# Performance work log

Hardware: AMD Instinct MI355X
Metric: run time of the kernel (lower is better)

Reference implementation:

```python
import jax, jax.numpy as jnp
import numpy as np
from jax import lax

BATCH, SEQ, IN_DIM, STATE, OUT_DIM = 8, 4096, 256, 256, 256


def setup_inputs() -> dict:
    key = jax.random.key(0)
    kx, ka, kb, kc = jax.random.split(key, 4)
    x = jax.random.normal(kx, (BATCH, SEQ, IN_DIM), dtype=jnp.float32)
    # A initialized as randn normalized by its largest singular value (spectral norm)
    A_init = jax.random.normal(ka, (STATE, STATE), dtype=jnp.float32)
    s_max = jnp.linalg.svd(A_init, compute_uv=False)[0]
    A = A_init / (s_max + 1e-8)
    B = jax.random.normal(kb, (IN_DIM, STATE), dtype=jnp.float32) / IN_DIM
    C = jax.random.normal(kc, (STATE, OUT_DIM), dtype=jnp.float32) / STATE
    h0 = jnp.zeros((STATE,), dtype=jnp.float32)
    return {"x": x, "A": A, "B": B, "C": C, "h0": h0}


def reference(x, A, B, C, h0):
    # h_{t} = h_{t-1} @ A + x_t @ B ;  y_t = h_t @ C
    bsz = x.shape[0]
    xB = jnp.einsum('bsi,in->sbn', x, B)  # precompute input projections, time-major
    h_init = jnp.broadcast_to(h0, (bsz, h0.shape[0]))

    def step(h, xb_t):
        h = h @ A + xb_t
        return h, h

    _, hs = lax.scan(step, h_init, xB)  # hs: [S, B, N]
    y = jnp.einsum('sbn,no->bso', hs, C)  # [B, S, O]
    return y
```

## Files before the change

### kernel.cpp

```cpp
#include <hip/hip_runtime.h>


#define SEQ    4096
#define NBATCH 8
#define ND     256
#define CHUNK  8
#define NCHUNK 512
#define GSZ    16
#define NGRP   32
#define LOSC   2048.0f
#define LOINV  (1.0f/2048.0f)

typedef _Float16 fp16_t;
typedef __attribute__((ext_vector_type(8))) _Float16 f16x8;
typedef __attribute__((ext_vector_type(4))) _Float16 f16x4;
typedef __attribute__((ext_vector_type(4))) float f32x4;

__global__ __launch_bounds__(64) void prep_frags3(
    const float* __restrict__ A, const float* __restrict__ B,
    const float* __restrict__ C,
    fp16_t* __restrict__ fAh, fp16_t* __restrict__ fAl,
    fp16_t* __restrict__ fBh, fp16_t* __restrict__ fBl,
    fp16_t* __restrict__ fCh, fp16_t* __restrict__ fCl) {
  const int which = blockIdx.x >> 7;
  const int blk   = blockIdx.x & 127;
  const float* M = (which == 0) ? A : (which == 1) ? B : C;
  fp16_t* hi = (which == 0) ? fAh : (which == 1) ? fBh : fCh;
  fp16_t* lo = (which == 0) ? fAl : (which == 1) ? fBl : fCl;
  const int lane = threadIdx.x;
  const int tile = blk >> 3, slice = blk & 7;
  const int n  = tile * 16 + (lane & 15);
  const int k0 = slice * 32 + (lane >> 4) * 8;
  f16x8 vh, vl;
  #pragma unroll
  for (int j = 0; j < 8; ++j) {
    const float v = M[(size_t)(k0 + j) * ND + n];
    const fp16_t h = (fp16_t)v;
    vh[j] = h;
    vl[j] = (fp16_t)((v - (float)h) * LOSC);
  }
  const size_t fo = ((size_t)blk * 64 + lane) * 8;
  *(f16x8*)&hi[fo] = vh;
  *(f16x8*)&lo[fo] = vl;
}

__global__ __launch_bounds__(64) void prep_frags2(
    const float* __restrict__ M0, const float* __restrict__ M1,
    fp16_t* __restrict__ h0p, fp16_t* __restrict__ l0p,
    fp16_t* __restrict__ h1p, fp16_t* __restrict__ l1p) {
  const int which = blockIdx.x >> 7;
  const int blk   = blockIdx.x & 127;
  const float* M = (which == 0) ? M0 : M1;
  fp16_t* hi = (which == 0) ? h0p : h1p;
  fp16_t* lo = (which == 0) ? l0p : l1p;
  const int lane = threadIdx.x;
  const int tile = blk >> 3, slice = blk & 7;
  const int n  = tile * 16 + (lane & 15);
  const int k0 = slice * 32 + (lane >> 4) * 8;
  f16x8 vh, vl;
  #pragma unroll
  for (int j = 0; j < 8; ++j) {
    const float v = M[(size_t)(k0 + j) * ND + n];
    const fp16_t h = (fp16_t)v;
    vh[j] = h;
    vl[j] = (fp16_t)((v - (float)h) * LOSC);
  }
  const size_t fo = ((size_t)blk * 64 + lane) * 8;
  *(f16x8*)&hi[fo] = vh;
  *(f16x8*)&lo[fo] = vl;
}

__global__ __launch_bounds__(1024, 2) void mfma_gemm(const float* __restrict__ X,
                                                     const fp16_t* __restrict__ Mhi,
                                                     const fp16_t* __restrict__ Mlo,
                                                     float* __restrict__ Out,
                                                     int mode) {
  const int m0   = blockIdx.x * 64;
  const int tid  = threadIdx.x;
  const int lane = tid & 63;
  const int w    = tid >> 6;
  const int br   = lane & 15;
  const int akg  = lane >> 4;

  __shared__ fp16_t Xh[32 * 512];
  __shared__ fp16_t Xl[32 * 512];
  char* Xhb = (char*)Xh;
  char* Xlb = (char*)Xl;

  #pragma unroll
  for (int pass = 0; pass < 2; ++pass) {
    const int tau = pass * 1024 + tid;
    const int row = tau >> 5;
    const int sub = tau & 31;
    const int s   = sub >> 2;
    const int ak  = sub & 3;
    const int m = m0 + row;
    const size_t in_row = (mode == 0)
        ? ((size_t)(m & 7) * SEQ + (m >> 3))
        : (size_t)m;
    const float* xp = &X[in_row * ND + s * 32 + ak * 8];
    const float4 x0 = *(const float4*)(xp);
    const float4 x1 = *(const float4*)(xp + 4);
    const float a[8] = {x0.x, x0.y, x0.z, x0.w, x1.x, x1.y, x1.z, x1.w};
    f16x8 vh, vl;
    #pragma unroll
    for (int j = 0; j < 8; ++j) {
      const fp16_t h = (fp16_t)a[j];
      vh[j] = h;
      vl[j] = (fp16_t)((a[j] - (float)h) * LOSC);
    }
    const int off = (((row >> 4) * 8 + s) << 10) +
                    (((ak << 4) | (row & 15)) ^ s) * 16;
    *(f16x8*)(Xhb + off) = vh;
    *(f16x8*)(Xlb + off) = vl;
  }

  f16x8 MH[8], ML[8];
  #pragma unroll
  for (int s = 0; s < 8; ++s) {
    const size_t fo = (((size_t)w * 8 + s) * 64 + lane) * 8;
    MH[s] = *(const f16x8*)&Mhi[fo];
    ML[s] = *(const f16x8*)&Mlo[fo];
  }
  __syncthreads();

  f32x4 accm[4], accl[4];
  #pragma unroll
  for (int mt = 0; mt < 4; ++mt) {
    accm[mt] = (f32x4)0.0f;
    accl[mt] = (f32x4)0.0f;
  }

  const int rdslot = (((akg << 4) | br)) * 16;
  #pragma unroll
  for (int s = 0; s < 8; ++s) {
    const int rdoff = (s ^ ((rdslot >> 4) & 0)) ;
    #pragma unroll
    for (int mt = 0; mt < 4; ++mt) {
      const int byte = ((mt * 8 + s) << 10) + ((((akg << 4) | br) ^ s) << 4);
      const f16x8 bh = *(const f16x8*)(Xhb + byte);
      const f16x8 bl = *(const f16x8*)(Xlb + byte);
      accm[mt] = __builtin_amdgcn_mfma_f32_16x16x32_f16(MH[s], bh, accm[mt], 0, 0, 0);
      accl[mt] = __builtin_amdgcn_mfma_f32_16x16x32_f16(ML[s], bh, accl[mt], 0, 0, 0);
      accl[mt] = __builtin_amdgcn_mfma_f32_16x16x32_f16(MH[s], bl, accl[mt], 0, 0, 0);
    }
    (void)rdoff;
  }

  #pragma unroll
  for (int mt = 0; mt < 4; ++mt) {
    const int m = m0 + mt * 16 + br;
    const size_t out_row = (mode == 1)
        ? ((size_t)(m & 7) * SEQ + (m >> 3))
        : (size_t)m;
    float4 o;
    o.x = accm[mt][0] + accl[mt][0] * LOINV;
    o.y = accm[mt][1] + accl[mt][1] * LOINV;
    o.z = accm[mt][2] + accl[mt][2] * LOINV;
    o.w = accm[mt][3] + accl[mt][3] * LOINV;
    *(float4*)&Out[out_row * ND + w * 16 + akg * 4] = o;
  }
}

__global__ __launch_bounds__(1024, 2) void mfma_rscan(
    const fp16_t* __restrict__ Mh, const fp16_t* __restrict__ Ml,
    const float* __restrict__ Init,
    const float* In,
    float* OutEach,
    float* __restrict__ OutFinal,
    int nupd, int gstride, int nseq, int init_bcast, int entry_mode) {
  const int seq0 = blockIdx.x * 2;
  const int tid  = threadIdx.x;
  const int lane = tid & 63;
  const int w    = tid >> 6;
  const int br   = lane & 15;
  const int akg  = lane >> 4;

  __shared__ fp16_t hH[2][8 * 512];
  __shared__ fp16_t hL[2][8 * 512];

  {
    const int task = tid >> 1;
    const int half = tid & 1;
    const int row  = task & 15;
    const int s    = (task >> 4) & 7;
    const int ak   = task >> 7;
    const int sq = seq0 + (row >> 3);
    const int b  = row & 7;
    const int c0 = s * 32 + ak * 8 + half * 4;
    float4 v = make_float4(0.f, 0.f, 0.f, 0.f);
    if (Init != nullptr && sq < nseq) {
      const size_t off = init_bcast ? (size_t)c0
                                    : ((size_t)sq * NBATCH + b) * ND + c0;
      v = *(const float4*)&Init[off];
      if (entry_mode && OutEach != nullptr)
        *(float4*)&OutEach[((size_t)sq * gstride * NBATCH + b) * ND + c0] = v;
    }
    const float a[4] = {v.x, v.y, v.z, v.w};
    f16x4 vh, vl;
    #pragma unroll
    for (int j = 0; j < 4; ++j) {
      const fp16_t h = (fp16_t)a[j];
      vh[j] = h;
      vl[j] = (fp16_t)((a[j] - (float)h) * LOSC);
    }
    const int off = (s << 10) + ((((ak << 4) | row) ^ s) << 4) + half * 8;
    *(f16x4*)((char*)hH[0] + off) = vh;
    *(f16x4*)((char*)hL[0] + off) = vl;
  }

  f16x8 AH[8], AL[8];
  #pragma unroll
  for (int s = 0; s < 8; ++s) {
    const size_t fo = (((size_t)w * 8 + s) * 64 + lane) * 8;
    AH[s] = *(const f16x8*)&Mh[fo];
    AL[s] = *(const f16x8*)&Ml[fo];
  }
  __syncthreads();

  const int sq   = seq0 + (br >> 3);
  const int b    = br & 7;
  const bool live = (sq < nseq);
  const int sqc  = live ? sq : (nseq - 1);
  const int col0 = w * 16 + akg * 4;

  int rdoff[8];
  #pragma unroll
  for (int s = 0; s < 8; ++s)
    rdoff[s] = (s << 10) + ((((akg << 4) | br) ^ s) << 4);
  const int sw   = col0 >> 5;
  const int akr  = (col0 >> 3) & 3;
  const int wroff = (sw << 10) + ((((akr << 4) | br) ^ sw) << 4) + (col0 & 7) * 2;

  float4 uv = *(const float4*)&In[((size_t)(sqc * gstride) * NBATCH + b) * ND + col0];
  float4 uvn;
  f32x4 res;
  int p = 0;
  for (int j = 0; j < nupd; ++j) {
    if (j + 1 < nupd)
      uvn = *(const float4*)&In[((size_t)(sqc * gstride + j + 1) * NBATCH + b) * ND + col0];
    const char* rH = (const char*)hH[p];
    const char* rL = (const char*)hL[p];
    f32x4 accm, acclA, acclB;
    accm[0] = uv.x; accm[1] = uv.y; accm[2] = uv.z; accm[3] = uv.w;
    acclA = (f32x4)0.0f;
    acclB = (f32x4)0.0f;
    #pragma unroll
    for (int s = 0; s < 8; ++s) {
      const f16x8 bh = *(const f16x8*)(rH + rdoff[s]);
      const f16x8 bl = *(const f16x8*)(rL + rdoff[s]);
      accm  = __builtin_amdgcn_mfma_f32_16x16x32_f16(AH[s], bh, accm,  0, 0, 0);
      acclA = __builtin_amdgcn_mfma_f32_16x16x32_f16(AL[s], bh, acclA, 0, 0, 0);
      acclB = __builtin_amdgcn_mfma_f32_16x16x32_f16(AH[s], bl, acclB, 0, 0, 0);
    }
    #pragma unroll
    for (int r = 0; r < 4; ++r) res[r] = accm[r] + (acclA[r] + acclB[r]) * LOINV;
    {
      f16x4 vh, vl;
      #pragma unroll
      for (int r = 0; r < 4; ++r) {
        const fp16_t hh = (fp16_t)res[r];
        vh[r] = hh;
        vl[r] = (fp16_t)((res[r] - (float)hh) * LOSC);
      }
      *(f16x4*)((char*)hH[p ^ 1] + wroff) = vh;
      *(f16x4*)((char*)hL[p ^ 1] + wroff) = vl;
    }
    if (OutEach != nullptr && live) {
      const size_t pos = entry_mode ? (size_t)(sq * gstride + j + 1)
                                    : (size_t)(sq * gstride + j);
      float4 o;
      o.x = res[0]; o.y = res[1]; o.z = res[2]; o.w = res[3];
      *(float4*)&OutEach[(pos * NBATCH + b) * ND + col0] = o;
    }
    uv = uvn;
    p ^= 1;
    __syncthreads();
  }

  if (OutFinal != nullptr && live) {
    float4 o;
    o.x = res[0]; o.y = res[1]; o.z = res[2]; o.w = res[3];
    *(float4*)&OutFinal[((size_t)sq * NBATCH + b) * ND + col0] = o;
  }
}

__global__ __launch_bounds__(256) void gemm256(const float* __restrict__ X,
                                               const float* __restrict__ Y,
                                               float* __restrict__ Out) {
  const int m0 = blockIdx.x * 4;
  const int n  = threadIdx.x;
  __shared__ float Xs[ND][4];
  #pragma unroll
  for (int r = 0; r < 4; ++r) Xs[n][r] = X[(m0 + r) * ND + n];
  __syncthreads();
  float a0 = 0.f, a1 = 0.f, a2 = 0.f, a3 = 0.f;
  #pragma unroll 8
  for (int k = 0; k < ND; ++k) {
    const float yv = Y[k * ND + n];
    const float4 xv = *(const float4*)&Xs[k][0];
    a0 = fmaf(xv.x, yv, a0);
    a1 = fmaf(xv.y, yv, a1);
    a2 = fmaf(xv.z, yv, a2);
    a3 = fmaf(xv.w, yv, a3);
  }
  Out[(m0 + 0) * ND + n] = a0;
  Out[(m0 + 1) * ND + n] = a1;
  Out[(m0 + 2) * ND + n] = a2;
  Out[(m0 + 3) * ND + n] = a3;
}

extern "C" void kernel_launch(void* const* d_in, const int* in_sizes, int n_in,
                              void* d_out, int out_size, void* d_ws, size_t ws_size,
                              hipStream_t stream) {
  const float* x  = (const float*)d_in[0];
  const float* A  = (const float*)d_in[1];
  const float* Bm = (const float*)d_in[2];
  const float* Cm = (const float*)d_in[3];
  const float* h0 = (const float*)d_in[4];
  float* y = (float*)d_out;

  float* U    = (float*)d_ws;
  float* t0   = U + (size_t)SEQ * NBATCH * ND;
  float* t1   = t0 + ND * ND;
  float* A8   = t1 + ND * ND;
  float* A128 = A8 + ND * ND;
  float* E    = A128 + ND * ND;
  float* Sg   = E + (size_t)NCHUNK * NBATCH * ND;
  float* G    = Sg + (size_t)NGRP * NBATCH * ND;
  float* Hc   = G + (size_t)NGRP * NBATCH * ND;
  fp16_t* fA_hi = (fp16_t*)(Hc + (size_t)NCHUNK * NBATCH * ND);
  fp16_t* fA_lo = fA_hi + ND * ND;
  fp16_t* fB_hi = fA_lo + ND * ND;
  fp16_t* fB_lo = fB_hi + ND * ND;
  fp16_t* fC_hi = fB_lo + ND * ND;
  fp16_t* fC_lo = fC_hi + ND * ND;
  fp16_t* fA8_hi   = (fp16_t*)t0;
  fp16_t* fA8_lo   = fA8_hi + ND * ND;
  fp16_t* fA128_hi = (fp16_t*)t1;
  fp16_t* fA128_lo = fA128_hi + ND * ND;

  prep_frags3<<<384, 64, 0, stream>>>(A, Bm, Cm, fA_hi, fA_lo, fB_hi, fB_lo,
                                      fC_hi, fC_lo);

  gemm256<<<64, 256, 0, stream>>>(A,  A,  t0);
  gemm256<<<64, 256, 0, stream>>>(t0, t0, t1);
  gemm256<<<64, 256, 0, stream>>>(t1, t1, A8);
  gemm256<<<64, 256, 0, stream>>>(A8, A8, t0);
  gemm256<<<64, 256, 0, stream>>>(t0, t0, t1);
  gemm256<<<64, 256, 0, stream>>>(t1, t1, t0);
  gemm256<<<64, 256, 0, stream>>>(t0, t0, A128);

  prep_frags2<<<256, 64, 0, stream>>>(A8, A128, fA8_hi, fA8_lo,
                                      fA128_hi, fA128_lo);

  mfma_gemm<<<512, 1024, 0, stream>>>(x, fB_hi, fB_lo, U, 0);

  mfma_rscan<<<NCHUNK / 2, 1024, 0, stream>>>(fA_hi, fA_lo, nullptr, U,
                                              nullptr, E, CHUNK, CHUNK,
                                              NCHUNK, 0, 0);

  mfma_rscan<<<NGRP / 2, 1024, 0, stream>>>(fA8_hi, fA8_lo, nullptr, E,
                                            nullptr, Sg, GSZ, GSZ, NGRP, 0, 0);

  mfma_rscan<<<1, 1024, 0, stream>>>(fA128_hi, fA128_lo, h0, Sg,
                                     G, nullptr, NGRP - 1, NGRP, 1, 1, 1);

  mfma_rscan<<<NGRP / 2, 1024, 0, stream>>>(fA8_hi, fA8_lo, G, E,
                                            Hc, nullptr, GSZ - 1, GSZ, NGRP,
                                            0, 1);

  mfma_rscan<<<NCHUNK / 2, 1024, 0, stream>>>(fA_hi, fA_lo, Hc, U,
                                              U, nullptr, CHUNK, CHUNK,
                                              NCHUNK, 0, 0);

  mfma_gemm<<<512, 1024, 0, stream>>>(U, fC_hi, fC_lo, y, 1);
}
```

Baseline: 232.9 us.

## Fuse input projection into chunk scan and output projection into down-sweep

Replaces the separate x@B GEMM plus first chunk scan with one scan_up kernel that computes each step's input projection with MFMA and immediately feeds the recurrence. Likewise, scan_down merges the final chunk rescan with the y=h@C projection, so hidden states never round-trip to global memory before the output GEMM. This drops two kernel launches and one full U read and write pass. In exchange each block holds twice as many fragment registers (A and B, or A and C), runs at one block per CU, and keeps the serial dependency on the per-step projection.

```diff
diff --git a/kernel.cpp b/kernel.cpp
--- a/kernel.cpp
+++ b/kernel.cpp
@@ -70,95 +70,298 @@
   *(f16x8*)&lo[fo] = vl;
 }
 
-__global__ __launch_bounds__(1024, 2) void mfma_gemm(const float* __restrict__ X,
-                                                     const fp16_t* __restrict__ Mhi,
-                                                     const fp16_t* __restrict__ Mlo,
-                                                     float* __restrict__ Out,
-                                                     int mode) {
-  const int m0   = blockIdx.x * 64;
+__global__ __launch_bounds__(1024, 1) void scan_up(
+    const fp16_t* __restrict__ fAh, const fp16_t* __restrict__ fAl,
+    const fp16_t* __restrict__ fBh, const fp16_t* __restrict__ fBl,
+    const float* __restrict__ x, float* __restrict__ U, float* __restrict__ E) {
+  const int c2   = blockIdx.x;
   const int tid  = threadIdx.x;
   const int lane = tid & 63;
   const int w    = tid >> 6;
   const int br   = lane & 15;
   const int akg  = lane >> 4;
 
-  __shared__ fp16_t Xh[32 * 512];
-  __shared__ fp16_t Xl[32 * 512];
-  char* Xhb = (char*)Xh;
-  char* Xlb = (char*)Xl;
-
-  #pragma unroll
-  for (int pass = 0; pass < 2; ++pass) {
-    const int tau = pass * 1024 + tid;
-    const int row = tau >> 5;
-    const int sub = tau & 31;
-    const int s   = sub >> 2;
-    const int ak  = sub & 3;
-    const int m = m0 + row;
-    const size_t in_row = (mode == 0)
-        ? ((size_t)(m & 7) * SEQ + (m >> 3))
-        : (size_t)m;
-    const float* xp = &X[in_row * ND + s * 32 + ak * 8];
-    const float4 x0 = *(const float4*)(xp);
-    const float4 x1 = *(const float4*)(xp + 4);
-    const float a[8] = {x0.x, x0.y, x0.z, x0.w, x1.x, x1.y, x1.z, x1.w};
-    f16x8 vh, vl;
-    #pragma unroll
-    for (int j = 0; j < 8; ++j) {
-      const fp16_t h = (fp16_t)a[j];
-      vh[j] = h;
-      vl[j] = (fp16_t)((a[j] - (float)h) * LOSC);
-    }
-    const int off = (((row >> 4) * 8 + s) << 10) +
-                    (((ak << 4) | (row & 15)) ^ s) * 16;
-    *(f16x8*)(Xhb + off) = vh;
-    *(f16x8*)(Xlb + off) = vl;
-  }
-
-  f16x8 MH[8], ML[8];
+  __shared__ fp16_t xH[2][8 * 512], xL[2][8 * 512];
+  __shared__ fp16_t hH[2][8 * 512], hL[2][8 * 512];
+
+  const int srow  = tid >> 6;
+  const int scol  = (tid & 63) * 4;
+  const int ss    = (tid >> 3) & 7;
+  const int sak   = (tid >> 1) & 3;
+  const int shalf = tid & 1;
+  const int soff  = (ss << 10) + ((((sak << 4) | srow) ^ ss) << 4) + shalf * 8;
+  const int sb    = srow & 7;
+  const int sc    = 2 * c2 + (srow >> 3);
+  const float* xsrc = &x[((size_t)sb * SEQ + (size_t)sc * CHUNK) * ND + scol];
+
+  f16x8 AH[8], AL[8], BH[8], BL[8];
   #pragma unroll
   for (int s = 0; s < 8; ++s) {
     const size_t fo = (((size_t)w * 8 + s) * 64 + lane) * 8;
-    MH[s] = *(const f16x8*)&Mhi[fo];
-    ML[s] = *(const f16x8*)&Mlo[fo];
+    AH[s] = *(const f16x8*)&fAh[fo];
+    AL[s] = *(const f16x8*)&fAl[fo];
+    BH[s] = *(const f16x8*)&fBh[fo];
+    BL[s] = *(const f16x8*)&fBl[fo];
+  }
+
+  {
+    const float4 xv = *(const float4*)xsrc;
+    const float a[4] = {xv.x, xv.y, xv.z, xv.w};
+    f16x4 vh, vl;
+    #pragma unroll
+    for (int r = 0; r < 4; ++r) {
+      const fp16_t h = (fp16_t)a[r];
+      vh[r] = h;
+      vl[r] = (fp16_t)((a[r] - (float)h) * LOSC);
+    }
+    *(f16x4*)((char*)xH[0] + soff) = vh;
+    *(f16x4*)((char*)xL[0] + soff) = vl;
   }
   __syncthreads();
 
-  f32x4 accm[4], accl[4];
-  #pragma unroll
-  for (int mt = 0; mt < 4; ++mt) {
-    accm[mt] = (f32x4)0.0f;
-    accl[mt] = (f32x4)0.0f;
-  }
-
-  const int rdslot = (((akg << 4) | br)) * 16;
+  const int sq   = 2 * c2 + (br >> 3);
+  const int b    = br & 7;
+  const int col0 = w * 16 + akg * 4;
+  int rdoff[8];
+  #pragma unroll
+  for (int s = 0; s < 8; ++s)
+    rdoff[s] = (s << 10) + ((((akg << 4) | br) ^ s) << 4);
+  const int sw    = col0 >> 5;
+  const int akr   = (col0 >> 3) & 3;
+  const int wroff = (sw << 10) + ((((akr << 4) | br) ^ sw) << 4) + (col0 & 7) * 2;
+
+  f32x4 res;
+  int q = 0, p = 0;
+  #pragma unroll 1
+  for (int j = 0; j < CHUNK; ++j) {
+    float4 xn;
+    if (j + 1 < CHUNK) xn = *(const float4*)(xsrc + (size_t)(j + 1) * ND);
+    f32x4 accm = (f32x4)0.0f, acclA = (f32x4)0.0f, acclB = (f32x4)0.0f;
+    {
+      const char* rH = (const char*)xH[q];
+      const char* rL = (const char*)xL[q];
+      #pragma unroll
+      for (int s = 0; s < 8; ++s) {
+        const f16x8 bh = *(const f16x8*)(rH + rdoff[s]);
+        const f16x8 bl = *(const f16x8*)(rL + rdoff[s]);
+        accm  = __builtin_amdgcn_mfma_f32_16x16x32_f16(BH[s], bh, accm,  0, 0, 0);
+        acclA = __builtin_amdgcn_mfma_f32_16x16x32_f16(BL[s], bh, acclA, 0, 0, 0);
+        acclB = __builtin_amdgcn_mfma_f32_16x16x32_f16(BH[s], bl, acclB, 0, 0, 0);
+      }
+    }
+    {
+      float4 o;
+      o.x = accm[0] + (acclA[0] + acclB[0]) * LOINV;
+      o.y = accm[1] + (acclA[1] + acclB[1]) * LOINV;
+      o.z = accm[2] + (acclA[2] + acclB[2]) * LOINV;
+      o.w = accm[3] + (acclA[3] + acclB[3]) * LOINV;
+      *(float4*)&U[((size_t)(sq * CHUNK + j) * NBATCH + b) * ND + col0] = o;
+    }
+    if (j > 0) {
+      const char* rH = (const char*)hH[p];
+      const char* rL = (const char*)hL[p];
+      #pragma unroll
+      for (int s = 0; s < 8; ++s) {
+        const f16x8 bh = *(const f16x8*)(rH + rdoff[s]);
+        const f16x8 bl = *(const f16x8*)(rL + rdoff[s]);
+        accm  = __builtin_amdgcn_mfma_f32_16x16x32_f16(AH[s], bh, accm,  0, 0, 0);
+        acclA = __builtin_amdgcn_mfma_f32_16x16x32_f16(AL[s], bh, acclA, 0, 0, 0);
+        acclB = __builtin_amdgcn_mfma_f32_16x16x32_f16(AH[s], bl, acclB, 0, 0, 0);
+      }
+    }
+    #pragma unroll
+    for (int r = 0; r < 4; ++r) res[r] = accm[r] + (acclA[r] + acclB[r]) * LOINV;
+    {
+      f16x4 vh, vl;
+      #pragma unroll
+      for (int r = 0; r < 4; ++r) {
+        const fp16_t hh = (fp16_t)res[r];
+        vh[r] = hh;
+        vl[r] = (fp16_t)((res[r] - (float)hh) * LOSC);
+      }
+      *(f16x4*)((char*)hH[p ^ 1] + wroff) = vh;
+      *(f16x4*)((char*)hL[p ^ 1] + wroff) = vl;
+    }
+    if (j + 1 < CHUNK) {
+      const float a[4] = {xn.x, xn.y, xn.z, xn.w};
+      f16x4 vh, vl;
+      #pragma unroll
+      for (int r = 0; r < 4; ++r) {
+        const fp16_t h = (fp16_t)a[r];
+        vh[r] = h;
+        vl[r] = (fp16_t)((a[r] - (float)h) * LOSC);
+      }
+      *(f16x4*)((char*)xH[q ^ 1] + soff) = vh;
+      *(f16x4*)((char*)xL[q ^ 1] + soff) = vl;
+    }
+    q ^= 1; p ^= 1;
+    __syncthreads();
+  }
+  {
+    float4 o;
+    o.x = res[0]; o.y = res[1]; o.z = res[2]; o.w = res[3];
+    *(float4*)&E[((size_t)sq * NBATCH + b) * ND + col0] = o;
+  }
+}
+
+__global__ __launch_bounds__(1024, 1) void scan_down(
+    const fp16_t* __restrict__ fAh, const fp16_t* __restrict__ fAl,
+    const fp16_t* __restrict__ fCh, const fp16_t* __restrict__ fCl,
+    const float* __restrict__ Hc, const float* __restrict__ U,
+    float* __restrict__ y) {
+  const int c2   = blockIdx.x;
+  const int tid  = threadIdx.x;
+  const int lane = tid & 63;
+  const int w    = tid >> 6;
+  const int br   = lane & 15;
+  const int akg  = lane >> 4;
+
+  __shared__ fp16_t hH[2][8 * 512], hL[2][8 * 512];
+
+  {
+    const int srow  = tid >> 6;
+    const int scol  = (tid & 63) * 4;
+    const int ss    = (tid >> 3) & 7;
+    const int sak   = (tid >> 1) & 3;
+    const int shalf = tid & 1;
+    const int soff  = (ss << 10) + ((((sak << 4) | srow) ^ ss) << 4) + shalf * 8;
+    const int sc = 2 * c2 + (srow >> 3);
+    const int sb = srow & 7;
+    const float4 v = *(const float4*)&Hc[((size_t)sc * NBATCH + sb) * ND + scol];
+    const float a[4] = {v.x, v.y, v.z, v.w};
+    f16x4 vh, vl;
+    #pragma unroll
+    for (int r = 0; r < 4; ++r) {
+      const fp16_t h = (fp16_t)a[r];
+      vh[r] = h;
+      vl[r] = (fp16_t)((a[r] - (float)h) * LOSC);
+    }
+    *(f16x4*)((char*)hH[0] + soff) = vh;
+    *(f16x4*)((char*)hL[0] + soff) = vl;
+  }
+
+  f16x8 AH[8], AL[8], CH[8], CL[8];
   #pragma unroll
   for (int s = 0; s < 8; ++s) {
-    const int rdoff = (s ^ ((rdslot >> 4) & 0)) ;
-    #pragma unroll
-    for (int mt = 0; mt < 4; ++mt) {
-      const int byte = ((mt * 8 + s) << 10) + ((((akg << 4) | br) ^ s) << 4);
-      const f16x8 bh = *(const f16x8*)(Xhb + byte);
-      const f16x8 bl = *(const f16x8*)(Xlb + byte);
-      accm[mt] = __builtin_amdgcn_mfma_f32_16x16x32_f16(MH[s], bh, accm[mt], 0, 0, 0);
-      accl[mt] = __builtin_amdgcn_mfma_f32_16x16x32_f16(ML[s], bh, accl[mt], 0, 0, 0);
-      accl[mt] = __builtin_amdgcn_mfma_f32_16x16x32_f16(MH[s], bl, accl[mt], 0, 0, 0);
-    }
-    (void)rdoff;
-  }
-
-  #pragma unroll
-  for (int mt = 0; mt < 4; ++mt) {
-    const int m = m0 + mt * 16 + br;
-    const size_t out_row = (mode == 1)
-        ? ((size_t)(m & 7) * SEQ + (m >> 3))
-        : (size_t)m;
+    const size_t fo = (((size_t)w * 8 + s) * 64 + lane) * 8;
+    AH[s] = *(const f16x8*)&fAh[fo];
+    AL[s] = *(const f16x8*)&fAl[fo];
+    CH[s] = *(const f16x8*)&fCh[fo];
+    CL[s] = *(const f16x8*)&fCl[fo];
+  }
+  __syncthreads();
+
+  const int sq   = 2 * c2 + (br >> 3);
+  const int b    = br & 7;
+  const int col0 = w * 16 + akg * 4;
+  int rdoff[8];
+  #pragma unroll
+  for (int s = 0; s < 8; ++s)
+    rdoff[s] = (s << 10) + ((((akg << 4) | br) ^ s) << 4);
+  const int sw    = col0 >> 5;
+  const int akr   = (col0 >> 3) & 3;
+  const int wroff = (sw << 10) + ((((akr << 4) | br) ^ sw) << 4) + (col0 & 7) * 2;
+  const size_t t0 = (size_t)sq * CHUNK;
+
+  float4 uv = *(const float4*)&U[(t0 * NBATCH + b) * ND + col0];
+  float4 uvn;
+  f32x4 res;
+  int p = 0;
+
+  {
+    uvn = *(const float4*)&U[((t0 + 1) * NBATCH + b) * ND + col0];
+    f32x4 accm, acclA = (f32x4)0.0f, acclB = (f32x4)0.0f;
+    accm[0] = uv.x; accm[1] = uv.y; accm[2] = uv.z; accm[3] = uv.w;
+    const char* rH = (const char*)hH[0];
+    const char* rL = (const char*)hL[0];
+    #pragma unroll
+    for (int s = 0; s < 8; ++s) {
+      const f16x8 bh = *(const f16x8*)(rH + rdoff[s]);
+      const f16x8 bl = *(const f16x8*)(rL + rdoff[s]);
+      accm  = __builtin_amdgcn_mfma_f32_16x16x32_f16(AH[s], bh, accm,  0, 0, 0);
+      acclA = __builtin_amdgcn_mfma_f32_16x16x32_f16(AL[s], bh, acclA, 0, 0, 0);
+      acclB = __builtin_amdgcn_mfma_f32_16x16x32_f16(AH[s], bl, acclB, 0, 0, 0);
+    }
+    #pragma unroll
+    for (int r = 0; r < 4; ++r) res[r] = accm[r] + (acclA[r] + acclB[r]) * LOINV;
+    f16x4 vh, vl;
+    #pragma unroll
+    for (int r = 0; r < 4; ++r) {
+      const fp16_t hh = (fp16_t)res[r];
+      vh[r] = hh;
+      vl[r] = (fp16_t)((res[r] - (float)hh) * LOSC);
+    }
+    *(f16x4*)((char*)hH[1] + wroff) = vh;
+    *(f16x4*)((char*)hL[1] + wroff) = vl;
+    uv = uvn;
+    p = 1;
+    __syncthreads();
+  }
+
+  #pragma unroll 1
+  for (int j = 1; j < CHUNK; ++j) {
+    if (j + 1 < CHUNK)
+      uvn = *(const float4*)&U[((t0 + j + 1) * NBATCH + b) * ND + col0];
+    f32x4 am, alA = (f32x4)0.0f, alB = (f32x4)0.0f;
+    f32x4 cm = (f32x4)0.0f, clA = (f32x4)0.0f, clB = (f32x4)0.0f;
+    am[0] = uv.x; am[1] = uv.y; am[2] = uv.z; am[3] = uv.w;
+    const char* rH = (const char*)hH[p];
+    const char* rL = (const char*)hL[p];
+    #pragma unroll
+    for (int s = 0; s < 8; ++s) {
+      const f16x8 bh = *(const f16x8*)(rH + rdoff[s]);
+      const f16x8 bl = *(const f16x8*)(rL + rdoff[s]);
+      am  = __builtin_amdgcn_mfma_f32_16x16x32_f16(AH[s], bh, am,  0, 0, 0);
+      alA = __builtin_amdgcn_mfma_f32_16x16x32_f16(AL[s], bh, alA, 0, 0, 0);
+      alB = __builtin_amdgcn_mfma_f32_16x16x32_f16(AH[s], bl, alB, 0, 0, 0);
+      cm  = __builtin_amdgcn_mfma_f32_16x16x32_f16(CH[s], bh, cm,  0, 0, 0);
+      clA = __builtin_amdgcn_mfma_f32_16x16x32_f16(CL[s], bh, clA, 0, 0, 0);
+      clB = __builtin_amdgcn_mfma_f32_16x16x32_f16(CH[s], bl, clB, 0, 0, 0);
+    }
+    #pragma unroll
+    for (int r = 0; r < 4; ++r) res[r] = am[r] + (alA[r] + alB[r]) * LOINV;
+    {
+      f16x4 vh, vl;
+      #pragma unroll
+      for (int r = 0; r < 4; ++r) {
+        const fp16_t hh = (fp16_t)res[r];
+        vh[r] = hh;
+        vl[r] = (fp16_t)((res[r] - (float)hh) * LOSC);
+      }
+      *(f16x4*)((char*)hH[p ^ 1] + wroff) = vh;
+      *(f16x4*)((char*)hL[p ^ 1] + wroff) = vl;
+    }
+    {
+      float4 o;
+      o.x = cm[0] + (clA[0] + clB[0]) * LOINV;
+      o.y = cm[1] + (clA[1] + clB[1]) * LOINV;
+      o.z = cm[2] + (clA[2] + clB[2]) * LOINV;
+      o.w = cm[3] + (clA[3] + clB[3]) * LOINV;
+      *(float4*)&y[((size_t)b * SEQ + t0 + j - 1) * ND + col0] = o;
+    }
+    uv = uvn;
+    p ^= 1;
+    __syncthreads();
+  }
+
+  {
+    f32x4 cm = (f32x4)0.0f, clA = (f32x4)0.0f, clB = (f32x4)0.0f;
+    const char* rH = (const char*)hH[p];
+    const char* rL = (const char*)hL[p];
+    #pragma unroll
+    for (int s = 0; s < 8; ++s) {
+      const f16x8 bh = *(const f16x8*)(rH + rdoff[s]);
+      const f16x8 bl = *(const f16x8*)(rL + rdoff[s]);
+      cm  = __builtin_amdgcn_mfma_f32_16x16x32_f16(CH[s], bh, cm,  0, 0, 0);
+      clA = __builtin_amdgcn_mfma_f32_16x16x32_f16(CL[s], bh, clA, 0, 0, 0);
+      clB = __builtin_amdgcn_mfma_f32_16x16x32_f16(CH[s], bl, clB, 0, 0, 0);
+    }
     float4 o;
-    o.x = accm[mt][0] + accl[mt][0] * LOINV;
-    o.y = accm[mt][1] + accl[mt][1] * LOINV;
-    o.z = accm[mt][2] + accl[mt][2] * LOINV;
-    o.w = accm[mt][3] + accl[mt][3] * LOINV;
-    *(float4*)&Out[out_row * ND + w * 16 + akg * 4] = o;
+    o.x = cm[0] + (clA[0] + clB[0]) * LOINV;
+    o.y = cm[1] + (clA[1] + clB[1]) * LOINV;
+    o.z = cm[2] + (clA[2] + clB[2]) * LOINV;
+    o.w = cm[3] + (clA[3] + clB[3]) * LOINV;
+    *(float4*)&y[((size_t)b * SEQ + t0 + CHUNK - 1) * ND + col0] = o;
   }
 }
 
@@ -354,11 +557,7 @@
   prep_frags2<<<256, 64, 0, stream>>>(A8, A128, fA8_hi, fA8_lo,
                                       fA128_hi, fA128_lo);
 
-  mfma_gemm<<<512, 1024, 0, stream>>>(x, fB_hi, fB_lo, U, 0);
-
-  mfma_rscan<<<NCHUNK / 2, 1024, 0, stream>>>(fA_hi, fA_lo, nullptr, U,
-                                              nullptr, E, CHUNK, CHUNK,
-                                              NCHUNK, 0, 0);
+  scan_up<<<NCHUNK / 2, 1024, 0, stream>>>(fA_hi, fA_lo, fB_hi, fB_lo, x, U, E);
 
   mfma_rscan<<<NGRP / 2, 1024, 0, stream>>>(fA8_hi, fA8_lo, nullptr, E,
                                             nullptr, Sg, GSZ, GSZ, NGRP, 0, 0);
@@ -370,9 +569,6 @@
                                             Hc, nullptr, GSZ - 1, GSZ, NGRP,
                                             0, 1);
 
-  mfma_rscan<<<NCHUNK / 2, 1024, 0, stream>>>(fA_hi, fA_lo, Hc, U,
-                                              U, nullptr, CHUNK, CHUNK,
-                                              NCHUNK, 0, 0);
-
-  mfma_gemm<<<512, 1024, 0, stream>>>(U, fC_hi, fC_lo, y, 1);
-}
+  scan_down<<<NCHUNK / 2, 1024, 0, stream>>>(fA_hi, fA_lo, fC_hi, fC_lo,
+                                             Hc, U, y);
+}
```

Result: slower. 320.0 us (+37.4%).
